# Performance work log

Hardware: AMD Instinct MI355X
Metric: run time of the kernel (lower is better)

## Reference

```python
import jax, jax.numpy as jnp
import numpy as np

B, T, E, H = 8, 2048, 1024, 64


def setup_inputs() -> dict:
    key = jax.random.key(0)
    kx, kq, kk, kv = jax.random.split(key, 4)
    x = jax.random.normal(kx, (B, T, E), dtype=jnp.float32)
    # nn.Linear(E, H, bias=False) weights, stored as (E, H) so y = x @ W
    scale = 0.02
    Wq = jax.random.normal(kq, (E, H), dtype=jnp.float32) * scale
    Wk = jax.random.normal(kk, (E, H), dtype=jnp.float32) * scale
    Wv = jax.random.normal(kv, (E, H), dtype=jnp.float32) * scale
    return {"x": x, "Wq": Wq, "Wk": Wk, "Wv": Wv}


def reference(x, Wq, Wk, Wv):
    # q, k, v: (B, T, H)
    q = x @ Wq
    k = x @ Wk
    v = x @ Wv
    # scores: (B, T, T)
    scores = jnp.einsum("btd,bsd->bts", q, k) / jnp.sqrt(jnp.asarray(H, q.dtype))
    # NOTE: the original module applies softmax over dim=0 (the batch dim).
    # With mask=None and is_decoder=False this is the only softmax applied.
    p = jax.nn.softmax(scores, axis=0)
    # output: (B, T, H)
    return jnp.einsum("bts,bsd->btd", p, v)
```

## Files before the change

### kernel.cpp

```cpp
#include <hip/hip_runtime.h>
#include <hip/hip_bf16.h>


typedef __attribute__((ext_vector_type(4))) float f32x4;
typedef __attribute__((ext_vector_type(4))) float float4_t;
typedef __attribute__((ext_vector_type(8))) short short8;
typedef __attribute__((ext_vector_type(4))) unsigned uint4_t;
typedef __attribute__((ext_vector_type(2))) unsigned uint2_t;

#define MFMA32(a, b, c) __builtin_amdgcn_mfma_f32_16x16x32_bf16(a, b, c, 0, 0, 0)

__device__ __forceinline__ short f2bf(float f) {
  unsigned u = __builtin_bit_cast(unsigned, f);
  unsigned r = (u + 0x7FFFu + ((u >> 16) & 1u)) >> 16;
  return (short)r;
}

__device__ __forceinline__ unsigned cvt_pk_bf16(float lo, float hi) {
  unsigned r;
  asm volatile("v_cvt_pk_bf16_f32 %0, %1, %2" : "=v"(r) : "v"(lo), "v"(hi));
  return r;
}

__device__ __forceinline__ void gload16(const short* g, short* l) {
  __builtin_amdgcn_global_load_lds(
      (const __attribute__((address_space(1))) unsigned*)g,
      (__attribute__((address_space(3))) unsigned*)l, 16, 0, 0);
}

__global__ __launch_bounds__(256) void wprep_kernel(
    const float* __restrict__ Wq, const float* __restrict__ Wk,
    const float* __restrict__ Wv, short* __restrict__ Wtb) {
  int lin = blockIdx.x * 256 + threadIdx.x;
  int l = lin & 63;
  int cf = (lin >> 6) % 12;
  int kt = lin / 768;
  int g = l >> 4, lr = l & 15;
  int wi = cf >> 2;
  int n = ((cf & 3) << 4) + lr;
  const float* W = (wi == 0) ? Wq : (wi == 1) ? Wk : Wv;
  short* dst = Wtb + (size_t)(kt * 12 + cf) * 512 + l * 8;
#pragma unroll
  for (int j = 0; j < 8; j++) dst[j] = f2bf(W[(kt * 32 + g * 8 + j) * 64 + n]);
}

__device__ __forceinline__ void proj_stage(const float* __restrict__ x,
                                           const short* __restrict__ Wtb,
                                           short* dst, int m0, int k0, int w, int l) {
  if (w < 4) {
#pragma unroll
    for (int i = 0; i < 5; i++) {
      int u = w * 5 + i;
      if (u < 8) {
        int ru = l >> 3, c = l & 7;
        const float* src =
            x + (size_t)(m0 + u * 8 + ru) * 1024 + k0 + ((c ^ ru) << 2);
        gload16((const short*)src, dst + u * 512);
      } else {
        int cf = u - 8;
        const short* src = Wtb + (size_t)((k0 >> 5) * 12 + cf) * 512 + l * 8;
        gload16(src, dst + u * 512);
      }
    }
  }
}

__device__ __forceinline__ void proj_compute(const short* __restrict__ ldsb,
                                             f32x4 (&acc)[6], int wr, int wc, int l) {
  const int g = l >> 4, lr = l & 15;
  const int ru = lr & 7;
  const int ub = (wr * 2 + (lr >> 3)) * 512;
  f32x4 fa = *(const f32x4*)&ldsb[ub + (ru * 8 + ((2 * g) ^ ru)) * 8];
  f32x4 fb = *(const f32x4*)&ldsb[ub + (ru * 8 + ((2 * g + 1) ^ ru)) * 8];
  uint4_t u_;
  u_[0] = cvt_pk_bf16(fa[0], fa[1]);
  u_[1] = cvt_pk_bf16(fa[2], fa[3]);
  u_[2] = cvt_pk_bf16(fb[0], fb[1]);
  u_[3] = cvt_pk_bf16(fb[2], fb[3]);
  short8 a = __builtin_bit_cast(short8, u_);
#pragma unroll
  for (int nf = 0; nf < 6; nf++) {
    int cf = wc * 6 + nf;
    short8 bfrag = *(const short8*)&ldsb[(8 + cf) * 512 + l * 8];
    acc[nf] = MFMA32(a, bfrag, acc[nf]);
  }
}

__global__ __launch_bounds__(512) void proj_kernel(
    const float* __restrict__ x, const short* __restrict__ Wtb,
    short* __restrict__ qb, short* __restrict__ kvb) {
  __shared__ __align__(16) short lds[4 * 20 * 512];
  const int tid = threadIdx.x;
  const int l = tid & 63, w = tid >> 6;
  const int g = l >> 4, lr = l & 15;
  const int wr = w & 3, wc = w >> 2;
  const int m0 = blockIdx.x * 64;

  f32x4 acc[6];
#pragma unroll
  for (int i = 0; i < 6; i++) acc[i] = (f32x4){0.f, 0.f, 0.f, 0.f};

  short* b0 = lds;
  short* b1 = lds + 10240;
  short* b2 = lds + 20480;
  short* b3 = lds + 30720;
  proj_stage(x, Wtb, b0, m0, 0, w, l);
  proj_stage(x, Wtb, b1, m0, 32, w, l);
  proj_stage(x, Wtb, b2, m0, 64, w, l);

  for (int I = 0; I < 30; I++) {
    asm volatile("s_waitcnt vmcnt(10)" ::: "memory");
    __builtin_amdgcn_s_barrier();
    __builtin_amdgcn_sched_barrier(0);
    if (I + 3 < 32) proj_stage(x, Wtb, b3, m0, (I + 3) * 32, w, l);
    proj_compute(b0, acc, wr, wc, l);
    short* t = b0; b0 = b1; b1 = b2; b2 = b3; b3 = t;
  }
  asm volatile("s_waitcnt vmcnt(5)" ::: "memory");
  __builtin_amdgcn_s_barrier();
  __builtin_amdgcn_sched_barrier(0);
  proj_compute(b0, acc, wr, wc, l);
  { short* t = b0; b0 = b1; b1 = b2; b2 = b3; b3 = t; }
  asm volatile("s_waitcnt vmcnt(0)" ::: "memory");
  __builtin_amdgcn_s_barrier();
  __builtin_amdgcn_sched_barrier(0);
  proj_compute(b0, acc, wr, wc, l);

#pragma unroll
  for (int nf = 0; nf < 6; nf++) {
    int colg0 = wc * 96 + nf * 16;
    int wi = colg0 >> 6;
    int d = (colg0 & 63) + lr;
    float scale = (wi == 0) ? 0.18033688f : 1.0f;
#pragma unroll
    for (int r = 0; r < 4; r++) {
      int row = m0 + wr * 16 + g * 4 + r;
      int b = row >> 11, t = row & 2047;
      short bv = f2bf(acc[nf][r] * scale);
      if (wi == 0) {
        int idx = (((b * 128 + (t >> 4)) * 2 + (d >> 5)) * 64 +
                   ((((d >> 3) & 3) << 4) | (t & 15))) * 8 + (d & 7);
        qb[idx] = bv;
      } else if (wi == 1) {
        int u = (b << 2) | (((t >> 4) & 1) << 1) | (d >> 5);
        int idx = (((t >> 5) * 64 + u) << 9) +
                  ((((((d >> 3) & 3) << 4)) | (t & 15)) << 3) + (d & 7);
        kvb[idx] = bv;
      } else {
        int u = 32 + (b << 2) + (d >> 4);
        int idx = (((t >> 5) * 64 + u) << 9) +
                  (((((t >> 2) & 3) << 4) | (d & 15)) << 3) + (((t >> 4) & 1) << 2) + (t & 3);
        kvb[idx] = bv;
      }
    }
  }
}

__device__ __forceinline__ void stage_step(const short* __restrict__ kvb,
                                           short* lds_buf, int w, int l, int W) {
#pragma unroll
  for (int i = 0; i < 8; i++) {
    int u = w * 8 + i;
    const short* src = kvb + (((size_t)W * 64 + u) << 9) + l * 8;
    gload16(src, lds_buf + u * 512);
  }
}

__global__ __launch_bounds__(512, 2) void attn_kernel(
    const short* __restrict__ qb, const short* __restrict__ kvb,
    short* __restrict__ partial) {
  __shared__ __align__(16) short lds[2][64 * 512];
  __shared__ __align__(16) uint2_t pxch[64 * 64];
  const int tid = threadIdx.x;
  const int l = tid & 63, w = tid >> 6;
  const int tt = w >> 1, dh = w & 1;
  const int lin = blockIdx.x;
  const int sc = lin & 7;
  const int tblk = lin >> 3;
  const int tb16 = tblk * 4 + tt;

  short8 qf[8][2];
#pragma unroll
  for (int b = 0; b < 8; b++)
#pragma unroll
    for (int ks = 0; ks < 2; ks++)
      qf[b][ks] = *(const short8*)&qb[(size_t)((b * 128 + tb16) * 2 + ks) * 512 + l * 8];

  f32x4 oacc[8][2];
#pragma unroll
  for (int b = 0; b < 8; b++)
#pragma unroll
    for (int n = 0; n < 2; n++) oacc[b][n] = (f32x4){0.f, 0.f, 0.f, 0.f};

  stage_step(kvb, &lds[0][0], w, l, sc * 8);

  for (int it = 0; it < 8; it++) {
    __syncthreads();
    if (it + 1 < 8) stage_step(kvb, &lds[(it + 1) & 1][0], w, l, sc * 8 + it + 1);
    const short* ldsc = &lds[it & 1][0];

    f32x4 S[8];
    __builtin_amdgcn_s_setprio(1);
#pragma unroll
    for (int b = 0; b < 8; b++) {
      short8 kf0 = *(const short8*)&ldsc[(b * 4 + dh * 2 + 0) * 512 + l * 8];
      short8 kf1 = *(const short8*)&ldsc[(b * 4 + dh * 2 + 1) * 512 + l * 8];
      f32x4 s = (f32x4){0.f, 0.f, 0.f, 0.f};
      s = MFMA32(kf0, qf[b][0], s);
      s = MFMA32(kf1, qf[b][1], s);
      S[b] = s;
    }
    __builtin_amdgcn_s_setprio(0);
#pragma unroll
    for (int r = 0; r < 4; r++) {
      float den = 0.f;
#pragma unroll
      for (int b = 0; b < 8; b++) {
        float e = __builtin_amdgcn_exp2f(S[b][r]);
        S[b][r] = e;
        den += e;
      }
      float inv = __builtin_amdgcn_rcpf(den);
#pragma unroll
      for (int b = 0; b < 8; b++) S[b][r] *= inv;
    }
    uint2_t pw[8];
#pragma unroll
    for (int b = 0; b < 8; b++) {
      pw[b][0] = cvt_pk_bf16(S[b][0], S[b][1]);
      pw[b][1] = cvt_pk_bf16(S[b][2], S[b][3]);
      pxch[(w * 8 + b) * 64 + l] = pw[b];
    }
    asm volatile("s_waitcnt lgkmcnt(0)" ::: "memory");
    __builtin_amdgcn_s_barrier();
    __builtin_amdgcn_sched_barrier(0);
    uint2_t pp[8];
#pragma unroll
    for (int b = 0; b < 8; b++) pp[b] = pxch[((w ^ 1) * 8 + b) * 64 + l];
    __builtin_amdgcn_s_setprio(1);
#pragma unroll
    for (int b = 0; b < 8; b++) {
      uint2_t lo = dh ? pp[b] : pw[b];
      uint2_t hi = dh ? pw[b] : pp[b];
      uint4_t pu;
      pu[0] = lo[0]; pu[1] = lo[1]; pu[2] = hi[0]; pu[3] = hi[1];
      short8 pbv = __builtin_bit_cast(short8, pu);
      short8 vf0 = *(const short8*)&ldsc[(32 + b * 4 + dh * 2 + 0) * 512 + l * 8];
      short8 vf1 = *(const short8*)&ldsc[(32 + b * 4 + dh * 2 + 1) * 512 + l * 8];
      oacc[b][0] = MFMA32(vf0, pbv, oacc[b][0]);
      oacc[b][1] = MFMA32(vf1, pbv, oacc[b][1]);
    }
    __builtin_amdgcn_s_setprio(0);
  }

  uint2_t* pout = (uint2_t*)partial;
#pragma unroll
  for (int b = 0; b < 8; b++)
#pragma unroll
    for (int n = 0; n < 2; n++) {
      int df = dh * 2 + n;
      uint2_t pk;
      pk[0] = cvt_pk_bf16(oacc[b][n][0], oacc[b][n][1]);
      pk[1] = cvt_pk_bf16(oacc[b][n][2], oacc[b][n][3]);
      pout[(size_t)(((sc * 8 + b) * 128 + tb16) * 4 + df) * 64 + l] = pk;
    }
}

__global__ __launch_bounds__(256) void reduce_kernel(const short* __restrict__ partial,
                                                     float* __restrict__ out) {
  int i = blockIdx.x * 256 + threadIdx.x;
  const uint2_t* p = (const uint2_t*)partial;
  float4_t a = (float4_t){0.f, 0.f, 0.f, 0.f};
  for (int sc = 0; sc < 8; sc++) {
    uint2_t v = p[(size_t)sc * 262144 + i];
    a[0] += __builtin_bit_cast(float, v[0] << 16);
    a[1] += __builtin_bit_cast(float, v[0] & 0xFFFF0000u);
    a[2] += __builtin_bit_cast(float, v[1] << 16);
    a[3] += __builtin_bit_cast(float, v[1] & 0xFFFF0000u);
  }
  int b = i >> 15;
  int r1 = i & 32767;
  int tb16 = r1 >> 8;
  int r2 = r1 & 255;
  int df = r2 >> 6;
  int ll = r2 & 63;
  int gg = ll >> 4, lrr = ll & 15;
  float4_t o = a;
  __builtin_nontemporal_store(
      o, (float4_t*)&out[(size_t)(b * 2048 + tb16 * 16 + lrr) * 64 + df * 16 + gg * 4]);
}

extern "C" void kernel_launch(void* const* d_in, const int* in_sizes, int n_in,
                              void* d_out, int out_size, void* d_ws, size_t ws_size,
                              hipStream_t stream) {
  const float* x = (const float*)d_in[0];
  const float* Wq = (const float*)d_in[1];
  const float* Wk = (const float*)d_in[2];
  const float* Wv = (const float*)d_in[3];
  float* out = (float*)d_out;

  char* ws = (char*)d_ws;
  short* qb = (short*)ws;
  short* kvb = qb + 16384 * 64;
  short* partial = kvb + 2 * 16384 * 64;
  short* Wtb = partial + 8ull * 262144 * 4;

  wprep_kernel<<<96, 256, 0, stream>>>(Wq, Wk, Wv, Wtb);
  proj_kernel<<<256, 512, 0, stream>>>(x, Wtb, qb, kvb);
  attn_kernel<<<256, 512, 0, stream>>>(qb, kvb, partial);
  reduce_kernel<<<1024, 256, 0, stream>>>(partial, out);
}
```

Measured before the change: 55.28 us.

## Double the projection k-step to 64 with a 3-stage pipeline using all waves

The projection GEMM pipeline now loads 64 k-elements per stage instead of 32, using all 8 waves for the global-to-LDS copies instead of only 4. It cuts the depth from 4 to 3 buffers and the iteration count from 32 to 16, so there are half as many barriers and waitcnt points per output tile. The cost is more LDS (120 KB total), which may limit occupancy, and a shallower prefetch distance in stages.

Measured after the change: 54.33 us (median of 2 runs). Within noise of the previous version (-1.7%).

```diff
diff --git a/kernel.cpp b/kernel.cpp
--- a/kernel.cpp
+++ b/kernel.cpp
@@ -47,20 +47,21 @@
 __device__ __forceinline__ void proj_stage(const float* __restrict__ x,
                                            const short* __restrict__ Wtb,
                                            short* dst, int m0, int k0, int w, int l) {
-  if (w < 4) {
-#pragma unroll
-    for (int i = 0; i < 5; i++) {
-      int u = w * 5 + i;
-      if (u < 8) {
-        int ru = l >> 3, c = l & 7;
-        const float* src =
-            x + (size_t)(m0 + u * 8 + ru) * 1024 + k0 + ((c ^ ru) << 2);
-        gload16((const short*)src, dst + u * 512);
-      } else {
-        int cf = u - 8;
-        const short* src = Wtb + (size_t)((k0 >> 5) * 12 + cf) * 512 + l * 8;
-        gload16(src, dst + u * 512);
-      }
+#pragma unroll
+  for (int i = 0; i < 5; i++) {
+    int u = w * 5 + i;
+    if (u < 16) {
+      int kh = u >> 3, ur = u & 7;
+      int ru = l >> 3, c = l & 7;
+      const float* src = x + (size_t)(m0 + ur * 8 + ru) * 1024 + k0 + kh * 32 +
+                         ((c ^ ru) << 2);
+      gload16((const short*)src, dst + u * 512);
+    } else {
+      int uu = u - 16;
+      int kh = uu / 12, cf = uu % 12;
+      const short* src =
+          Wtb + (size_t)(((k0 >> 5) + kh) * 12 + cf) * 512 + l * 8;
+      gload16(src, dst + u * 512);
     }
   }
 }
@@ -69,27 +70,30 @@
                                              f32x4 (&acc)[6], int wr, int wc, int l) {
   const int g = l >> 4, lr = l & 15;
   const int ru = lr & 7;
-  const int ub = (wr * 2 + (lr >> 3)) * 512;
-  f32x4 fa = *(const f32x4*)&ldsb[ub + (ru * 8 + ((2 * g) ^ ru)) * 8];
-  f32x4 fb = *(const f32x4*)&ldsb[ub + (ru * 8 + ((2 * g + 1) ^ ru)) * 8];
-  uint4_t u_;
-  u_[0] = cvt_pk_bf16(fa[0], fa[1]);
-  u_[1] = cvt_pk_bf16(fa[2], fa[3]);
-  u_[2] = cvt_pk_bf16(fb[0], fb[1]);
-  u_[3] = cvt_pk_bf16(fb[2], fb[3]);
-  short8 a = __builtin_bit_cast(short8, u_);
-#pragma unroll
-  for (int nf = 0; nf < 6; nf++) {
-    int cf = wc * 6 + nf;
-    short8 bfrag = *(const short8*)&ldsb[(8 + cf) * 512 + l * 8];
-    acc[nf] = MFMA32(a, bfrag, acc[nf]);
+#pragma unroll
+  for (int kh = 0; kh < 2; kh++) {
+    const int ub = (kh * 8 + wr * 2 + (lr >> 3)) * 512;
+    f32x4 fa = *(const f32x4*)&ldsb[ub + (ru * 8 + ((2 * g) ^ ru)) * 8];
+    f32x4 fb = *(const f32x4*)&ldsb[ub + (ru * 8 + ((2 * g + 1) ^ ru)) * 8];
+    uint4_t u_;
+    u_[0] = cvt_pk_bf16(fa[0], fa[1]);
+    u_[1] = cvt_pk_bf16(fa[2], fa[3]);
+    u_[2] = cvt_pk_bf16(fb[0], fb[1]);
+    u_[3] = cvt_pk_bf16(fb[2], fb[3]);
+    short8 a = __builtin_bit_cast(short8, u_);
+#pragma unroll
+    for (int nf = 0; nf < 6; nf++) {
+      int cf = wc * 6 + nf;
+      short8 bfrag = *(const short8*)&ldsb[(16 + kh * 12 + cf) * 512 + l * 8];
+      acc[nf] = MFMA32(a, bfrag, acc[nf]);
+    }
   }
 }
 
 __global__ __launch_bounds__(512) void proj_kernel(
     const float* __restrict__ x, const short* __restrict__ Wtb,
     short* __restrict__ qb, short* __restrict__ kvb) {
-  __shared__ __align__(16) short lds[4 * 20 * 512];
+  __shared__ __align__(16) short lds[3 * 40 * 512];
   const int tid = threadIdx.x;
   const int l = tid & 63, w = tid >> 6;
   const int g = l >> 4, lr = l & 15;
@@ -100,31 +104,18 @@
 #pragma unroll
   for (int i = 0; i < 6; i++) acc[i] = (f32x4){0.f, 0.f, 0.f, 0.f};
 
-  short* b0 = lds;
-  short* b1 = lds + 10240;
-  short* b2 = lds + 20480;
-  short* b3 = lds + 30720;
-  proj_stage(x, Wtb, b0, m0, 0, w, l);
-  proj_stage(x, Wtb, b1, m0, 32, w, l);
-  proj_stage(x, Wtb, b2, m0, 64, w, l);
-
-  for (int I = 0; I < 30; I++) {
-    asm volatile("s_waitcnt vmcnt(10)" ::: "memory");
+  proj_stage(x, Wtb, lds, m0, 0, w, l);
+  proj_stage(x, Wtb, lds + 20480, m0, 64, w, l);
+
+  for (int I = 0; I < 16; I++) {
+    if (I < 15) { asm volatile("s_waitcnt vmcnt(5)" ::: "memory"); }
+    else        { asm volatile("s_waitcnt vmcnt(0)" ::: "memory"); }
     __builtin_amdgcn_s_barrier();
     __builtin_amdgcn_sched_barrier(0);
-    if (I + 3 < 32) proj_stage(x, Wtb, b3, m0, (I + 3) * 32, w, l);
-    proj_compute(b0, acc, wr, wc, l);
-    short* t = b0; b0 = b1; b1 = b2; b2 = b3; b3 = t;
-  }
-  asm volatile("s_waitcnt vmcnt(5)" ::: "memory");
-  __builtin_amdgcn_s_barrier();
-  __builtin_amdgcn_sched_barrier(0);
-  proj_compute(b0, acc, wr, wc, l);
-  { short* t = b0; b0 = b1; b1 = b2; b2 = b3; b3 = t; }
-  asm volatile("s_waitcnt vmcnt(0)" ::: "memory");
-  __builtin_amdgcn_s_barrier();
-  __builtin_amdgcn_sched_barrier(0);
-  proj_compute(b0, acc, wr, wc, l);
+    if (I + 2 < 16)
+      proj_stage(x, Wtb, lds + ((I + 2) % 3) * 20480, m0, (I + 2) * 64, w, l);
+    proj_compute(lds + (I % 3) * 20480, acc, wr, wc, l);
+  }
 
 #pragma unroll
   for (int nf = 0; nf < 6; nf++) {
```
